# Optimization experiments

Measured on AMD Instinct MI355X. Metric: run time of the kernel, lower is better.

Reference implementation:

```python
import jax, jax.numpy as jnp
import numpy as np

D_MODEL = 512
NHEAD = 8
D_K = D_MODEL // NHEAD


def setup_inputs() -> dict:
    key = jax.random.key(0)
    ks = jax.random.split(key, 9)
    s = 1.0 / np.sqrt(D_MODEL)
    x = jax.random.normal(ks[0], (2, 2048, D_MODEL), dtype=jnp.float32)
    # torch Linear weights: [out_features, in_features]
    Wq = jax.random.uniform(ks[1], (D_MODEL, D_MODEL), jnp.float32, -s, s)
    bq = jax.random.uniform(ks[2], (D_MODEL,), jnp.float32, -s, s)
    Wk = jax.random.uniform(ks[3], (D_MODEL, D_MODEL), jnp.float32, -s, s)
    bk = jax.random.uniform(ks[4], (D_MODEL,), jnp.float32, -s, s)
    Wv = jax.random.uniform(ks[5], (D_MODEL, D_MODEL), jnp.float32, -s, s)
    bv = jax.random.uniform(ks[6], (D_MODEL,), jnp.float32, -s, s)
    Wo = jax.random.uniform(ks[7], (D_MODEL, D_MODEL), jnp.float32, -s, s)
    bo = jax.random.uniform(ks[8], (D_MODEL,), jnp.float32, -s, s)
    return {"x": x, "Wq": Wq, "bq": bq, "Wk": Wk, "bk": bk,
            "Wv": Wv, "bv": bv, "Wo": Wo, "bo": bo}


def reference(x, Wq, bq, Wk, bk, Wv, bv, Wo, bo):
    B, S, D = x.shape
    H, Dk = NHEAD, D_K

    def proj(W, b):
        # torch Linear: x @ W.T + b -> [B, S, D] -> [B, H, S, Dk]
        y = jnp.einsum('bsd,ed->bse', x, W) + b
        return y.reshape(B, S, H, Dk).transpose(0, 2, 1, 3)

    q = proj(Wq, bq)
    k = proj(Wk, bk)
    v = proj(Wv, bv)

    scores = jnp.einsum('bhqd,bhkd->bhqk', q, k) / jnp.sqrt(jnp.float32(Dk))
    attn = jax.nn.softmax(scores, axis=-1)  # explicit O(S^2) attention matrix
    out = jnp.einsum('bhqk,bhkd->bhqd', attn, v)
    out = out.transpose(0, 2, 1, 3).reshape(B, S, D)
    return jnp.einsum('bsd,ed->bse', out, Wo) + bo
```

## Files before the change

### kernel.cpp

```cpp
#include <hip/hip_runtime.h>

typedef __bf16 bf16_t;
typedef bf16_t bf16x8 __attribute__((ext_vector_type(8)));
typedef bf16_t bf16x4 __attribute__((ext_vector_type(4)));
typedef float  floatx4 __attribute__((ext_vector_type(4)));
typedef short  s16x4   __attribute__((ext_vector_type(4)));

#define D_MODEL 512
#define NHEAD   8
#define DK      64
#define BATCH   2
#define SEQ     2048
#define MTOT    (BATCH*SEQ)
#define QSCALE  0.18033688011112042591f

static __device__ __forceinline__ floatx4 mfma16(bf16x8 a, bf16x8 b, floatx4 c) {
    return __builtin_amdgcn_mfma_f32_16x16x32_bf16(a, b, c, 0, 0, 0);
}
static __device__ __forceinline__ floatx4 mfma16k16(s16x4 a, s16x4 b, floatx4 c) {
    return __builtin_amdgcn_mfma_f32_16x16x16bf16_1k(a, b, c, 0, 0, 0);
}

static __device__ __forceinline__ void glds16(bf16_t* lds, const bf16_t* g) {
    __builtin_amdgcn_global_load_lds(
        (const __attribute__((address_space(1))) unsigned int*)g,
        (__attribute__((address_space(3))) unsigned int*)lds,
        16, 0, 0);
}

__global__ __launch_bounds__(256)
void to_bf16(const float* __restrict__ x,
             const float* __restrict__ Wq, const float* __restrict__ Wk,
             const float* __restrict__ Wv, const float* __restrict__ Wo,
             bf16_t* __restrict__ xb, bf16_t* __restrict__ wqb,
             bf16_t* __restrict__ wkb, bf16_t* __restrict__ wvb,
             bf16_t* __restrict__ wob)
{
    const int blk = blockIdx.x;
    const float* src; bf16_t* dst; size_t base;
    if      (blk < 1024) { src = x;  dst = xb;  base = (size_t)blk * 2048; }
    else if (blk < 1152) { src = Wq; dst = wqb; base = (size_t)(blk - 1024) * 2048; }
    else if (blk < 1280) { src = Wk; dst = wkb; base = (size_t)(blk - 1152) * 2048; }
    else if (blk < 1408) { src = Wv; dst = wvb; base = (size_t)(blk - 1280) * 2048; }
    else                 { src = Wo; dst = wob; base = (size_t)(blk - 1408) * 2048; }
    const size_t off = base + (size_t)threadIdx.x * 8;
    const float4 a = *(const float4*)(src + off);
    const float4 b = *(const float4*)(src + off + 4);
    bf16x8 p;
    p[0]=(bf16_t)a.x; p[1]=(bf16_t)a.y; p[2]=(bf16_t)a.z; p[3]=(bf16_t)a.w;
    p[4]=(bf16_t)b.x; p[5]=(bf16_t)b.y; p[6]=(bf16_t)b.z; p[7]=(bf16_t)b.w;
    const size_t off2 = off ^ ((((off >> 10) & 3)) << 3);
    *(bf16x8*)(dst + off2) = p;
}

__global__ __launch_bounds__(256)
void qkv_proj(const bf16_t* __restrict__ xb,
              const bf16_t* __restrict__ wqb, const float* __restrict__ bq,
              const bf16_t* __restrict__ wkb, const float* __restrict__ bk,
              const bf16_t* __restrict__ wvb, const float* __restrict__ bv,
              bf16_t* __restrict__ q_ws, bf16_t* __restrict__ k_ws,
              bf16_t* __restrict__ vt_ws)
{
    __shared__ bf16_t As[2][64 * 32];
    __shared__ bf16_t Bs[2][128 * 32];

    const int mtile = blockIdx.x;
    const int ntile = blockIdx.y;
    const int which = ntile >> 2;
    const int nsub  = ntile & 3;
    const bf16_t* W   = (which == 0) ? wqb : (which == 1) ? wkb : wvb;
    const float* bias = (which == 0) ? bq  : (which == 1) ? bk  : bv;

    const int tid  = threadIdx.x;
    const int lane = tid & 63;
    const int wave = tid >> 6;
    const int wm = wave & 1, wn = wave >> 1;
    const int l15 = lane & 15, quad = lane >> 4;
    const int m0 = mtile * 64;
    const int n0 = nsub * 128;
    const int lr = lane >> 2;
    const int lc = (lane & 3) * 8;
    const int csw = (quad ^ ((l15 >> 1) & 3)) * 8;

    floatx4 acc[2][4] = {};

    {
        glds16(&As[0][wave * 16 * 32], xb + (size_t)(m0 + wave * 16 + lr) * 512 + lc);
        #pragma unroll
        for (int q = 0; q < 2; ++q) {
            const int r = wave * 32 + q * 16;
            glds16(&Bs[0][r * 32], W + (size_t)(n0 + r + lr) * 512 + lc);
        }
    }

    for (int kk = 0; kk < 16; ++kk) {
        const int buf = kk & 1;
        __syncthreads();
        if (kk < 15) {
            const int kn = (kk + 1) * 32;
            glds16(&As[buf ^ 1][wave * 16 * 32],
                   xb + (size_t)(m0 + wave * 16 + lr) * 512 + kn + lc);
            #pragma unroll
            for (int q = 0; q < 2; ++q) {
                const int r = wave * 32 + q * 16;
                glds16(&Bs[buf ^ 1][r * 32], W + (size_t)(n0 + r + lr) * 512 + kn + lc);
            }
        }

        bf16x8 af[2], bfr[4];
        #pragma unroll
        for (int i = 0; i < 2; ++i)
            af[i] = *(const bf16x8*)(&As[buf][(wm * 32 + i * 16 + l15) * 32 + csw]);
        #pragma unroll
        for (int j = 0; j < 4; ++j)
            bfr[j] = *(const bf16x8*)(&Bs[buf][(wn * 64 + j * 16 + l15) * 32 + csw]);
        #pragma unroll
        for (int i = 0; i < 2; ++i)
            #pragma unroll
            for (int j = 0; j < 4; ++j)
                acc[i][j] = mfma16(af[i], bfr[j], acc[i][j]);
    }

    #pragma unroll
    for (int j = 0; j < 4; ++j) {
        const int e = n0 + wn * 64 + j * 16 + l15;
        const float be = bias[e];
        const int h = e >> 6, d = e & 63;
        #pragma unroll
        for (int i = 0; i < 2; ++i) {
            const int mbase = m0 + wm * 32 + i * 16 + quad * 4;
            const int b = mbase >> 11;
            const int sl = mbase & 2047;
            floatx4 c = acc[i][j];
            if (which == 2) {
                bf16x4 pk;
                #pragma unroll
                for (int r = 0; r < 4; ++r) pk[r] = (bf16_t)(c[r] + be);
                const int slz = (sl & ~63) | ((((sl >> 3) & 7) ^ (d & 7)) << 3) | (sl & 7);
                *(bf16x4*)(vt_ws + ((size_t)((b * 8 + h) * 64 + d)) * 2048 + slz) = pk;
            } else if (which == 1) {
                #pragma unroll
                for (int r = 0; r < 4; ++r) {
                    const int s = sl + r;
                    const int dz = ((((d >> 3) ^ (s & 7))) << 3) | (d & 7);
                    k_ws[(size_t)(b * 8 + h) * (SEQ * DK) + (size_t)s * 64 + dz] =
                        (bf16_t)(c[r] + be);
                }
            } else {
                #pragma unroll
                for (int r = 0; r < 4; ++r)
                    q_ws[(size_t)(b * 8 + h) * (SEQ * DK) + (size_t)(sl + r) * 64 + d] =
                        (bf16_t)((c[r] + be) * QSCALE);
            }
        }
    }
}

__global__ __launch_bounds__(256, 2)
void attn_kernel(const bf16_t* __restrict__ q_ws, const bf16_t* __restrict__ k_ws,
                 const bf16_t* __restrict__ vt_ws, bf16_t* __restrict__ attn_ws)
{
    __shared__ bf16_t Kt[2][2][64 * 64];
    __shared__ bf16_t Vt[2][2][64 * 64];

    const int bh = blockIdx.x;
    const int qt = blockIdx.y;
    const int tid = threadIdx.x, lane = tid & 63, wave = tid >> 6;
    const int l15 = lane & 15, quad = lane >> 4;
    const int g  = wave >> 1;
    const int wq = wave & 1;

    const bf16_t* Qb  = q_ws  + (size_t)bh * SEQ * DK;
    const bf16_t* Kb  = k_ws  + (size_t)bh * SEQ * DK;
    const bf16_t* Vtb = vt_ws + (size_t)bh * DK * SEQ;

    const int sp = wave & 1;
    const bool isK = wave < 2;
    const int srow8 = lane >> 3;
    const int scol  = (lane & 7) * 8;

    bf16x8 aq[2][2];
    #pragma unroll
    for (int mt = 0; mt < 2; ++mt)
        #pragma unroll
        for (int c = 0; c < 2; ++c)
            aq[mt][c] = *(const bf16x8*)(Qb +
                (size_t)(qt * 64 + wq * 32 + mt * 16 + l15) * 64 + c * 32 + quad * 8);

    floatx4 O[2][4] = {};
    float rs[2] = {0.f, 0.f};
    const int ksw0 = ((0 + quad) ^ (l15 & 7)) * 8;
    const int ksw1 = ((4 + quad) ^ (l15 & 7)) * 8;

    {
        const int kg = sp * 64;
        bf16_t* stile = isK ? &Kt[0][sp][0] : &Vt[0][sp][0];
        if (isK) {
            #pragma unroll
            for (int i = 0; i < 8; ++i)
                glds16(stile + i * 512, Kb + (size_t)(kg + i * 8 + srow8) * 64 + scol);
        } else {
            #pragma unroll
            for (int i = 0; i < 8; ++i)
                glds16(stile + i * 512, Vtb + (size_t)(i * 8 + srow8) * 2048 + kg + scol);
        }
    }

    for (int t = 0; t < 16; ++t) {
        const int buf = t & 1;
        __syncthreads();
        if (t < 15) {
            const int kg = (t + 1) * 128 + sp * 64;
            bf16_t* stile = isK ? &Kt[buf ^ 1][sp][0] : &Vt[buf ^ 1][sp][0];
            if (isK) {
                #pragma unroll
                for (int i = 0; i < 8; ++i)
                    glds16(stile + i * 512, Kb + (size_t)(kg + i * 8 + srow8) * 64 + scol);
            } else {
                #pragma unroll
                for (int i = 0; i < 8; ++i)
                    glds16(stile + i * 512, Vtb + (size_t)(i * 8 + srow8) * 2048 + kg + scol);
            }
        }

        s16x4 pf[2][4];
        #pragma unroll
        for (int kf = 0; kf < 4; ++kf) {
            const bf16_t* krow = &Kt[buf][g][(kf * 16 + l15) * 64];
            bf16x8 k0 = *(const bf16x8*)(krow + ksw0);
            bf16x8 k1 = *(const bf16x8*)(krow + ksw1);
            #pragma unroll
            for (int mt = 0; mt < 2; ++mt) {
                floatx4 z = {0.f, 0.f, 0.f, 0.f};
                z = mfma16(k0, aq[mt][0], z);
                z = mfma16(k1, aq[mt][1], z);
                bf16x4 pk;
                float s = 0.f;
                #pragma unroll
                for (int r = 0; r < 4; ++r) {
                    const float p = __builtin_amdgcn_exp2f(z[r]);
                    s += p;
                    pk[r] = (bf16_t)p;
                }
                rs[mt] += s;
                pf[mt][kf] = __builtin_bit_cast(s16x4, pk);
            }
        }

        #pragma unroll
        for (int kg2 = 0; kg2 < 4; ++kg2) {
            const int voff = (((kg2 * 2 + (quad >> 1)) ^ (l15 & 7)) * 8) + (quad & 1) * 4;
            #pragma unroll
            for (int df = 0; df < 4; ++df) {
                const s16x4 v = *(const s16x4*)(&Vt[buf][g][(df * 16 + l15) * 64 + voff]);
                #pragma unroll
                for (int mt = 0; mt < 2; ++mt)
                    O[mt][df] = mfma16k16(pf[mt][kg2], v, O[mt][df]);
            }
        }
    }

    #pragma unroll
    for (int mt = 0; mt < 2; ++mt) {
        rs[mt] += __shfl_xor(rs[mt], 16, 64);
        rs[mt] += __shfl_xor(rs[mt], 32, 64);
    }

    float* scratch = (float*)&Kt[0][0][0];
    __syncthreads();
    if (g == 1) {
        float* s = scratch + (size_t)(wq * 64 + lane) * 35;
        #pragma unroll
        for (int mt = 0; mt < 2; ++mt) {
            #pragma unroll
            for (int df = 0; df < 4; ++df)
                #pragma unroll
                for (int r = 0; r < 4; ++r) s[mt * 16 + df * 4 + r] = O[mt][df][r];
            s[32 + mt] = rs[mt];
        }
    }
    __syncthreads();
    if (g == 0) {
        const float* s = scratch + (size_t)(wq * 64 + lane) * 35;
        #pragma unroll
        for (int mt = 0; mt < 2; ++mt) {
            #pragma unroll
            for (int df = 0; df < 4; ++df)
                #pragma unroll
                for (int r = 0; r < 4; ++r) O[mt][df][r] += s[mt * 16 + df * 4 + r];
            rs[mt] += s[32 + mt];
        }

        const int b = bh >> 3, h = bh & 7;
        #pragma unroll
        for (int mt = 0; mt < 2; ++mt)
            #pragma unroll
            for (int r = 0; r < 4; ++r) {
                const float rv = __shfl(rs[mt], (quad << 4) + ((quad & 3) << 2) + r, 64);
                const float rinv = 1.0f / rv;
                const int s_ = qt * 64 + wq * 32 + mt * 16 + quad * 4 + r;
                const int sw = ((s_ >> 1) & 3) << 3;
                const size_t base = ((size_t)b * 2048 + s_) * 512;
                #pragma unroll
                for (int df = 0; df < 4; ++df) {
                    const int col = h * 64 + df * 16 + l15;
                    attn_ws[base + (col ^ sw)] = (bf16_t)(O[mt][df][r] * rinv);
                }
            }
    }
}

__global__ __launch_bounds__(256)
void out_proj(const bf16_t* __restrict__ attn_ws, const bf16_t* __restrict__ wob,
              const float* __restrict__ bo, float* __restrict__ y)
{
    __shared__ bf16_t As[2][64 * 32];
    __shared__ bf16_t Bs[2][128 * 32];

    const int mtile = blockIdx.x;
    const int ntile = blockIdx.y;
    const int tid = threadIdx.x, lane = tid & 63, wave = tid >> 6;
    const int wm = wave & 1, wn = wave >> 1;
    const int l15 = lane & 15, quad = lane >> 4;
    const int m0 = mtile * 64;
    const int n0 = ntile * 128;
    const int lr = lane >> 2, lc = (lane & 3) * 8;
    const int csw = (quad ^ ((l15 >> 1) & 3)) * 8;

    floatx4 acc[2][4] = {};

    {
        glds16(&As[0][wave * 16 * 32], attn_ws + (size_t)(m0 + wave * 16 + lr) * 512 + lc);
        #pragma unroll
        for (int q = 0; q < 2; ++q) {
            const int r = wave * 32 + q * 16;
            glds16(&Bs[0][r * 32], wob + (size_t)(n0 + r + lr) * 512 + lc);
        }
    }

    for (int kk = 0; kk < 16; ++kk) {
        const int buf = kk & 1;
        __syncthreads();
        if (kk < 15) {
            const int kn = (kk + 1) * 32;
            glds16(&As[buf ^ 1][wave * 16 * 32],
                   attn_ws + (size_t)(m0 + wave * 16 + lr) * 512 + kn + lc);
            #pragma unroll
            for (int q = 0; q < 2; ++q) {
                const int r = wave * 32 + q * 16;
                glds16(&Bs[buf ^ 1][r * 32], wob + (size_t)(n0 + r + lr) * 512 + kn + lc);
            }
        }

        bf16x8 af[2], bfr[4];
        #pragma unroll
        for (int i = 0; i < 2; ++i)
            af[i] = *(const bf16x8*)(&As[buf][(wm * 32 + i * 16 + l15) * 32 + csw]);
        #pragma unroll
        for (int j = 0; j < 4; ++j)
            bfr[j] = *(const bf16x8*)(&Bs[buf][(wn * 64 + j * 16 + l15) * 32 + csw]);
        #pragma unroll
        for (int i = 0; i < 2; ++i)
            #pragma unroll
            for (int j = 0; j < 4; ++j)
                acc[i][j] = mfma16(af[i], bfr[j], acc[i][j]);
    }

    #pragma unroll
    for (int j = 0; j < 4; ++j) {
        const int e = n0 + wn * 64 + j * 16 + l15;
        const float be = bo[e];
        #pragma unroll
        for (int i = 0; i < 2; ++i) {
            const int mb = m0 + wm * 32 + i * 16 + quad * 4;
            #pragma unroll
            for (int r = 0; r < 4; ++r)
                y[(size_t)(mb + r) * 512 + e] = acc[i][j][r] + be;
        }
    }
}

extern "C" void kernel_launch(void* const* d_in, const int* in_sizes, int n_in,
                              void* d_out, int out_size, void* d_ws, size_t ws_size,
                              hipStream_t stream) {
    (void)in_sizes; (void)n_in; (void)out_size; (void)ws_size;
    const float* x  = (const float*)d_in[0];
    const float* Wq = (const float*)d_in[1];
    const float* bq = (const float*)d_in[2];
    const float* Wk = (const float*)d_in[3];
    const float* bk = (const float*)d_in[4];
    const float* Wv = (const float*)d_in[5];
    const float* bv = (const float*)d_in[6];
    const float* Wo = (const float*)d_in[7];
    const float* bo = (const float*)d_in[8];

    bf16_t* xb   = (bf16_t*)d_ws;
    bf16_t* wqb  = xb   + (size_t)MTOT * D_MODEL;
    bf16_t* wkb  = wqb  + (size_t)D_MODEL * D_MODEL;
    bf16_t* wvb  = wkb  + (size_t)D_MODEL * D_MODEL;
    bf16_t* wob  = wvb  + (size_t)D_MODEL * D_MODEL;
    bf16_t* qws  = wob  + (size_t)D_MODEL * D_MODEL;
    bf16_t* kws  = qws  + (size_t)MTOT * D_MODEL;
    bf16_t* vtws = kws  + (size_t)MTOT * D_MODEL;
    bf16_t* aws  = vtws + (size_t)MTOT * D_MODEL;

    to_bf16    <<<1536, 256, 0, stream>>>(x, Wq, Wk, Wv, Wo, xb, wqb, wkb, wvb, wob);
    qkv_proj   <<<dim3(64, 12), 256, 0, stream>>>(xb, wqb, bq, wkb, bk, wvb, bv, qws, kws, vtws);
    attn_kernel<<<dim3(16, 32), 256, 0, stream>>>(qws, kws, vtws, aws);
    out_proj   <<<dim3(64, 4),  256, 0, stream>>>(aws, wob, bo, (float*)d_out);
}
```

Baseline: 129.4 us.

## Fuse fp32-to-bf16 conversion into projection GEMM loads, drop to_bf16 kernel

Removes the separate to_bf16 conversion kernel. The QKV and output projection GEMMs now read fp32 x and weights directly into registers, convert them to bf16, and store them swizzled into LDS, using a two-deep register prefetch in place of direct global-to-LDS loads. This saves one launch and a round trip of the converted activations and weights through memory. In exchange, each GEMM reads twice as many bytes per element, the weights are converted again by every tile, and a second barrier is added per k-step.

```diff
diff --git a/kernel.cpp b/kernel.cpp
--- a/kernel.cpp
+++ b/kernel.cpp
@@ -20,44 +20,24 @@
 static __device__ __forceinline__ floatx4 mfma16k16(s16x4 a, s16x4 b, floatx4 c) {
     return __builtin_amdgcn_mfma_f32_16x16x16bf16_1k(a, b, c, 0, 0, 0);
 }
-
 static __device__ __forceinline__ void glds16(bf16_t* lds, const bf16_t* g) {
     __builtin_amdgcn_global_load_lds(
         (const __attribute__((address_space(1))) unsigned int*)g,
         (__attribute__((address_space(3))) unsigned int*)lds,
         16, 0, 0);
 }
-
-__global__ __launch_bounds__(256)
-void to_bf16(const float* __restrict__ x,
-             const float* __restrict__ Wq, const float* __restrict__ Wk,
-             const float* __restrict__ Wv, const float* __restrict__ Wo,
-             bf16_t* __restrict__ xb, bf16_t* __restrict__ wqb,
-             bf16_t* __restrict__ wkb, bf16_t* __restrict__ wvb,
-             bf16_t* __restrict__ wob)
-{
-    const int blk = blockIdx.x;
-    const float* src; bf16_t* dst; size_t base;
-    if      (blk < 1024) { src = x;  dst = xb;  base = (size_t)blk * 2048; }
-    else if (blk < 1152) { src = Wq; dst = wqb; base = (size_t)(blk - 1024) * 2048; }
-    else if (blk < 1280) { src = Wk; dst = wkb; base = (size_t)(blk - 1152) * 2048; }
-    else if (blk < 1408) { src = Wv; dst = wvb; base = (size_t)(blk - 1280) * 2048; }
-    else                 { src = Wo; dst = wob; base = (size_t)(blk - 1408) * 2048; }
-    const size_t off = base + (size_t)threadIdx.x * 8;
-    const float4 a = *(const float4*)(src + off);
-    const float4 b = *(const float4*)(src + off + 4);
+static __device__ __forceinline__ bf16x8 cvt8(float4 a, float4 b) {
     bf16x8 p;
     p[0]=(bf16_t)a.x; p[1]=(bf16_t)a.y; p[2]=(bf16_t)a.z; p[3]=(bf16_t)a.w;
     p[4]=(bf16_t)b.x; p[5]=(bf16_t)b.y; p[6]=(bf16_t)b.z; p[7]=(bf16_t)b.w;
-    const size_t off2 = off ^ ((((off >> 10) & 3)) << 3);
-    *(bf16x8*)(dst + off2) = p;
+    return p;
 }
 
 __global__ __launch_bounds__(256)
-void qkv_proj(const bf16_t* __restrict__ xb,
-              const bf16_t* __restrict__ wqb, const float* __restrict__ bq,
-              const bf16_t* __restrict__ wkb, const float* __restrict__ bk,
-              const bf16_t* __restrict__ wvb, const float* __restrict__ bv,
+void qkv_proj(const float* __restrict__ x,
+              const float* __restrict__ Wq, const float* __restrict__ bq,
+              const float* __restrict__ Wk, const float* __restrict__ bk,
+              const float* __restrict__ Wv, const float* __restrict__ bv,
               bf16_t* __restrict__ q_ws, bf16_t* __restrict__ k_ws,
               bf16_t* __restrict__ vt_ws)
 {
@@ -68,8 +48,8 @@
     const int ntile = blockIdx.y;
     const int which = ntile >> 2;
     const int nsub  = ntile & 3;
-    const bf16_t* W   = (which == 0) ? wqb : (which == 1) ? wkb : wvb;
-    const float* bias = (which == 0) ? bq  : (which == 1) ? bk  : bv;
+    const float* W    = (which == 0) ? Wq : (which == 1) ? Wk : Wv;
+    const float* bias = (which == 0) ? bq : (which == 1) ? bk : bv;
 
     const int tid  = threadIdx.x;
     const int lane = tid & 63;
@@ -78,33 +58,46 @@
     const int l15 = lane & 15, quad = lane >> 4;
     const int m0 = mtile * 64;
     const int n0 = nsub * 128;
-    const int lr = lane >> 2;
-    const int lc = (lane & 3) * 8;
     const int csw = (quad ^ ((l15 >> 1) & 3)) * 8;
 
+    const int arow = tid >> 2, aseg = tid & 3;
+    const int brow = tid >> 1, bsg0 = (tid & 1) * 2;
+    const int aswz = (arow >> 1) & 3;
+    const int bswz = (brow >> 1) & 3;
+    const float* pa = x + (size_t)(m0 + arow) * 512 + aseg * 8;
+    const float* pb = W + (size_t)(n0 + brow) * 512 + bsg0 * 8;
+
+    float4 ra[2][2], rb[2][4];
+    #pragma unroll
+    for (int bank = 0; bank < 2; ++bank) {
+        const int k0 = bank * 32;
+        ra[bank][0] = *(const float4*)(pa + k0);
+        ra[bank][1] = *(const float4*)(pa + k0 + 4);
+        rb[bank][0] = *(const float4*)(pb + k0);
+        rb[bank][1] = *(const float4*)(pb + k0 + 4);
+        rb[bank][2] = *(const float4*)(pb + k0 + 8);
+        rb[bank][3] = *(const float4*)(pb + k0 + 12);
+    }
+
     floatx4 acc[2][4] = {};
-
-    {
-        glds16(&As[0][wave * 16 * 32], xb + (size_t)(m0 + wave * 16 + lr) * 512 + lc);
-        #pragma unroll
-        for (int q = 0; q < 2; ++q) {
-            const int r = wave * 32 + q * 16;
-            glds16(&Bs[0][r * 32], W + (size_t)(n0 + r + lr) * 512 + lc);
-        }
-    }
 
     for (int kk = 0; kk < 16; ++kk) {
         const int buf = kk & 1;
+        *(bf16x8*)(&As[buf][arow * 32 + (aseg ^ aswz) * 8]) =
+            cvt8(ra[buf][0], ra[buf][1]);
+        *(bf16x8*)(&Bs[buf][brow * 32 + (bsg0 ^ bswz) * 8]) =
+            cvt8(rb[buf][0], rb[buf][1]);
+        *(bf16x8*)(&Bs[buf][brow * 32 + ((bsg0 + 1) ^ bswz) * 8]) =
+            cvt8(rb[buf][2], rb[buf][3]);
         __syncthreads();
-        if (kk < 15) {
-            const int kn = (kk + 1) * 32;
-            glds16(&As[buf ^ 1][wave * 16 * 32],
-                   xb + (size_t)(m0 + wave * 16 + lr) * 512 + kn + lc);
-            #pragma unroll
-            for (int q = 0; q < 2; ++q) {
-                const int r = wave * 32 + q * 16;
-                glds16(&Bs[buf ^ 1][r * 32], W + (size_t)(n0 + r + lr) * 512 + kn + lc);
-            }
+        if (kk < 14) {
+            const int k0 = (kk + 2) * 32;
+            ra[buf][0] = *(const float4*)(pa + k0);
+            ra[buf][1] = *(const float4*)(pa + k0 + 4);
+            rb[buf][0] = *(const float4*)(pb + k0);
+            rb[buf][1] = *(const float4*)(pb + k0 + 4);
+            rb[buf][2] = *(const float4*)(pb + k0 + 8);
+            rb[buf][3] = *(const float4*)(pb + k0 + 12);
         }
 
         bf16x8 af[2], bfr[4];
@@ -119,6 +112,7 @@
             #pragma unroll
             for (int j = 0; j < 4; ++j)
                 acc[i][j] = mfma16(af[i], bfr[j], acc[i][j]);
+        __syncthreads();
     }
 
     #pragma unroll
@@ -311,7 +305,7 @@
 }
 
 __global__ __launch_bounds__(256)
-void out_proj(const bf16_t* __restrict__ attn_ws, const bf16_t* __restrict__ wob,
+void out_proj(const bf16_t* __restrict__ attn_ws, const float* __restrict__ Wo,
               const float* __restrict__ bo, float* __restrict__ y)
 {
     __shared__ bf16_t As[2][64 * 32];
@@ -324,32 +318,43 @@
     const int l15 = lane & 15, quad = lane >> 4;
     const int m0 = mtile * 64;
     const int n0 = ntile * 128;
-    const int lr = lane >> 2, lc = (lane & 3) * 8;
     const int csw = (quad ^ ((l15 >> 1) & 3)) * 8;
 
+    const int arow = tid >> 2, aseg = tid & 3;
+    const int brow = tid >> 1, bsg0 = (tid & 1) * 2;
+    const int bswz = (brow >> 1) & 3;
+    const bf16_t* pa = attn_ws + (size_t)(m0 + arow) * 512 + aseg * 8;
+    const float*  pb = Wo + (size_t)(n0 + brow) * 512 + bsg0 * 8;
+
+    bf16x8 ra[2];
+    float4 rb[2][4];
+    #pragma unroll
+    for (int bank = 0; bank < 2; ++bank) {
+        const int k0 = bank * 32;
+        ra[bank] = *(const bf16x8*)(pa + k0);
+        rb[bank][0] = *(const float4*)(pb + k0);
+        rb[bank][1] = *(const float4*)(pb + k0 + 4);
+        rb[bank][2] = *(const float4*)(pb + k0 + 8);
+        rb[bank][3] = *(const float4*)(pb + k0 + 12);
+    }
+
     floatx4 acc[2][4] = {};
-
-    {
-        glds16(&As[0][wave * 16 * 32], attn_ws + (size_t)(m0 + wave * 16 + lr) * 512 + lc);
-        #pragma unroll
-        for (int q = 0; q < 2; ++q) {
-            const int r = wave * 32 + q * 16;
-            glds16(&Bs[0][r * 32], wob + (size_t)(n0 + r + lr) * 512 + lc);
-        }
-    }
 
     for (int kk = 0; kk < 16; ++kk) {
         const int buf = kk & 1;
+        *(bf16x8*)(&As[buf][arow * 32 + aseg * 8]) = ra[buf];
+        *(bf16x8*)(&Bs[buf][brow * 32 + (bsg0 ^ bswz) * 8]) =
+            cvt8(rb[buf][0], rb[buf][1]);
+        *(bf16x8*)(&Bs[buf][brow * 32 + ((bsg0 + 1) ^ bswz) * 8]) =
+            cvt8(rb[buf][2], rb[buf][3]);
         __syncthreads();
-        if (kk < 15) {
-            const int kn = (kk + 1) * 32;
-            glds16(&As[buf ^ 1][wave * 16 * 32],
-                   attn_ws + (size_t)(m0 + wave * 16 + lr) * 512 + kn + lc);
-            #pragma unroll
-            for (int q = 0; q < 2; ++q) {
-                const int r = wave * 32 + q * 16;
-                glds16(&Bs[buf ^ 1][r * 32], wob + (size_t)(n0 + r + lr) * 512 + kn + lc);
-            }
+        if (kk < 14) {
+            const int k0 = (kk + 2) * 32;
+            ra[buf] = *(const bf16x8*)(pa + k0);
+            rb[buf][0] = *(const float4*)(pb + k0);
+            rb[buf][1] = *(const float4*)(pb + k0 + 4);
+            rb[buf][2] = *(const float4*)(pb + k0 + 8);
+            rb[buf][3] = *(const float4*)(pb + k0 + 12);
         }
 
         bf16x8 af[2], bfr[4];
@@ -364,6 +369,7 @@
             #pragma unroll
             for (int j = 0; j < 4; ++j)
                 acc[i][j] = mfma16(af[i], bfr[j], acc[i][j]);
+        __syncthreads();
     }
 
     #pragma unroll
@@ -394,18 +400,12 @@
     const float* Wo = (const float*)d_in[7];
     const float* bo = (const float*)d_in[8];
 
-    bf16_t* xb   = (bf16_t*)d_ws;
-    bf16_t* wqb  = xb   + (size_t)MTOT * D_MODEL;
-    bf16_t* wkb  = wqb  + (size_t)D_MODEL * D_MODEL;
-    bf16_t* wvb  = wkb  + (size_t)D_MODEL * D_MODEL;
-    bf16_t* wob  = wvb  + (size_t)D_MODEL * D_MODEL;
-    bf16_t* qws  = wob  + (size_t)D_MODEL * D_MODEL;
+    bf16_t* qws  = (bf16_t*)d_ws;
     bf16_t* kws  = qws  + (size_t)MTOT * D_MODEL;
     bf16_t* vtws = kws  + (size_t)MTOT * D_MODEL;
     bf16_t* aws  = vtws + (size_t)MTOT * D_MODEL;
 
-    to_bf16    <<<1536, 256, 0, stream>>>(x, Wq, Wk, Wv, Wo, xb, wqb, wkb, wvb, wob);
-    qkv_proj   <<<dim3(64, 12), 256, 0, stream>>>(xb, wqb, bq, wkb, bk, wvb, bv, qws, kws, vtws);
+    qkv_proj   <<<dim3(64, 12), 256, 0, stream>>>(x, Wq, bq, Wk, bk, Wv, bv, qws, kws, vtws);
     attn_kernel<<<dim3(16, 32), 256, 0, stream>>>(qws, kws, vtws, aws);
-    out_proj   <<<dim3(64, 4),  256, 0, stream>>>(aws, wob, bo, (float*)d_out);
-}
+    out_proj   <<<dim3(64, 4),  256, 0, stream>>>(aws, Wo, bo, (float*)d_out);
+}
```

Measured after the change: 132.6 us. 2.5% more time.
